# Optimization experiments

Measured on AMD Instinct MI355X. Metric: run time of the kernel, lower is better.

Reference implementation:

```python
import jax, jax.numpy as jnp
import numpy as np

K = 3          # kernel size
STRIDE = 2
PAD = 1
DIL = 1
SHAPE = 128    # input spatial extent per axis
B = 2          # batch size
N = 100000     # active input voxels
CIN = 32
COUT = 64
OUT = (SHAPE + 2 * PAD - DIL * (K - 1) - 1) // STRIDE + 1  # 64


def setup_inputs() -> dict:
    key = jax.random.key(0)
    kf, kw, kc, kb = jax.random.split(key, 4)
    features = jax.random.normal(kf, (N, CIN), jnp.float32)
    W = jax.random.normal(kw, (K, K, K, CIN, COUT), jnp.float32) * 0.05
    xyz = jax.random.randint(kc, (N, 3), 0, SHAPE, jnp.int32)
    b = jax.random.randint(kb, (N, 1), 0, B, jnp.int32)
    coors = jnp.concatenate([b, xyz], axis=1)  # [N, 4] = (batch, z, y, x)
    return {"features": features, "W": W, "coors": coors, "batch_size": B}


def reference(features, W, coors, batch_size):
    # Sparse 3D conv via gather-GEMM-scatter per kernel offset.
    # Output voxel o receives input p iff p = o*stride - pad + k*dil, i.e.
    # o = (p + pad - k*dil) / stride when divisible and in range.
    bidx = coors[:, 0].astype(jnp.int32)          # [N]
    pos = coors[:, 1:4].astype(jnp.int32)         # [N, 3]
    out = jnp.zeros((batch_size * OUT * OUT * OUT, COUT), features.dtype)
    for kz in range(K):
        for ky in range(K):
            for kx in range(K):
                off = jnp.array([kz, ky, kx], jnp.int32)
                num = pos + PAD - off * DIL        # [N, 3]
                o = num // STRIDE                  # candidate output coords
                valid = jnp.all((num % STRIDE == 0) & (o >= 0) & (o < OUT), axis=1)
                flat = ((bidx * OUT + o[:, 0]) * OUT + o[:, 1]) * OUT + o[:, 2]
                flat = jnp.where(valid, flat, 0)
                contrib = jnp.where(valid[:, None], features, 0.0) @ W[kz, ky, kx]
                out = out.at[flat].add(contrib)
    # Densified sparse-conv output: active sites hold exact spconv values,
    # inactive sites are zero (no contributions).
    return out.reshape(batch_size, OUT, OUT, OUT, COUT)
```

## Files before the change

kernel.cpp:

```cpp
#include <hip/hip_runtime.h>


#define CIN   32
#define COUT  64
#define OUTD  64
#define NBLK  2048
#define NPTS  128

__device__ __forceinline__ int axis_opts(int p, int* k, int* o) {
    int cnt = 0;
    const int kp = (p + 1) & 1;
    const int o0 = (p + 1 - kp) >> 1;
    if (o0 < OUTD) { k[cnt] = kp; o[cnt] = o0; ++cnt; }
    if (kp == 0) {
        const int o1 = o0 - 1;
        if (o1 >= 0) { k[cnt] = 2; o[cnt] = o1; ++cnt; }
    }
    return cnt;
}

__global__ void conv_w_bf16(const float* __restrict__ W, ushort* __restrict__ wsW)
{
    const int k = blockIdx.x;
    for (int i = threadIdx.x; i < CIN * COUT; i += 256) {
        const int c = i >> 6, ch = i & 63;
        const unsigned u = __float_as_uint(W[k * CIN * COUT + i]);
        const unsigned r = (u + 0x7fffu + ((u >> 16) & 1u)) >> 16;
        wsW[(k << 11) + (ch << 5) + c] = (ushort)r;
    }
}

__global__ __launch_bounds__(256) void scatter2(
    const float* __restrict__ feats, const ushort* __restrict__ wsW,
    const int4* __restrict__ coors, float* __restrict__ out,
    int N, int totWaves)
{
    const int ch = threadIdx.x & 63;
    const int wv = __builtin_amdgcn_readfirstlane(threadIdx.x >> 6);
    const int gwave = blockIdx.x * 4 + wv;

    for (int i = gwave; i < N; i += totWaves) {
        const int4 c = coors[i];
        const float4* fp = (const float4*)(feats + (size_t)i * CIN);
        float4 f[8];
        #pragma unroll
        for (int q = 0; q < 8; ++q) f[q] = fp[q];

        int kz[2], oz[2], ky[2], oy[2], kx[2], ox[2];
        const int nz = axis_opts(c.y, kz, oz);
        const int ny = axis_opts(c.z, ky, oy);
        const int nx = axis_opts(c.w, kx, ox);

        for (int az = 0; az < nz; ++az)
        for (int ay = 0; ay < ny; ++ay)
        for (int ax = 0; ax < nx; ++ax) {
            const int kidx = (kz[az] * 3 + ky[ay]) * 3 + kx[ax];
            const uint4* wp = (const uint4*)(wsW + (kidx << 11) + (ch << 5));
            uint4 w4[4];
            #pragma unroll
            for (int q = 0; q < 4; ++q) w4[q] = wp[q];
            float s0 = 0.f, s1 = 0.f;
            #pragma unroll
            for (int q = 0; q < 4; ++q) {
                const uint4 wq = w4[q];
                const float4 fa = f[2 * q], fb = f[2 * q + 1];
                s0 += fa.x * __uint_as_float(wq.x << 16);
                s1 += fa.y * __uint_as_float(wq.x & 0xffff0000u);
                s0 += fa.z * __uint_as_float(wq.y << 16);
                s1 += fa.w * __uint_as_float(wq.y & 0xffff0000u);
                s0 += fb.x * __uint_as_float(wq.z << 16);
                s1 += fb.y * __uint_as_float(wq.z & 0xffff0000u);
                s0 += fb.z * __uint_as_float(wq.w << 16);
                s1 += fb.w * __uint_as_float(wq.w & 0xffff0000u);
            }
            const size_t flat = (((size_t)c.x * OUTD + oz[az]) * OUTD + oy[ay]) * OUTD + ox[ax];
            unsafeAtomicAdd(out + flat * COUT + ch, s0 + s1);
        }
    }
}

__global__ __launch_bounds__(256, 4) void spconv_scatter(
    const float* __restrict__ feats, const float* __restrict__ Wt,
    const int* __restrict__ coors, float* __restrict__ out, int N)
{
    __shared__ float sf[NPTS][CIN];
    __shared__ int   sc[NPTS][4];
    __shared__ int   vf[NPTS];

    const int tid = threadIdx.x;
    const int ch  = tid & 63;
    const int wv  = tid >> 6;
    const int base = blockIdx.x * NPTS;
    const int npts = min(NPTS, (int)(N - base));
    if (npts <= 0) return;

    for (int i = tid; i < npts * CIN; i += 256) sf[0][i] = feats[base * CIN + i];
    for (int i = tid; i < npts * 4; i += 256) ((int*)sc)[i] = coors[base * 4 + i];
    __syncthreads();

    for (int off = 0; off < 27; ++off) {
        const int kz = off / 9, ky = (off / 3) % 3, kx = off % 3;
        if (tid < npts) {
            const int p  = tid;
            const int nz = sc[p][1] + 1 - kz;
            const int ny = sc[p][2] + 1 - ky;
            const int nx = sc[p][3] + 1 - kx;
            const int m  = nz | ny | nx;
            const int oz = nz >> 1, oy = ny >> 1, ox = nx >> 1;
            const bool v = ((m & 0x80000001) == 0) &&
                           (oz < OUTD) && (oy < OUTD) && (ox < OUTD);
            vf[p] = v ? (((sc[p][0] * OUTD + oz) * OUTD + oy) * OUTD + ox) : -1;
        }
        const float* wp = Wt + off * (CIN * COUT) + ch;
        float w[CIN];
        #pragma unroll
        for (int c = 0; c < CIN; ++c) w[c] = wp[c * COUT];
        __syncthreads();
        for (int p = wv; p < npts; p += 4) {
            const int f = vf[p];
            if (f >= 0) {
                float s = 0.f;
                #pragma unroll
                for (int c = 0; c < CIN; ++c) s += sf[p][c] * w[c];
                atomicAdd(&out[(size_t)f * COUT + ch], s);
            }
        }
        __syncthreads();
    }
}

extern "C" void kernel_launch(void* const* d_in, const int* in_sizes, int n_in,
                              void* d_out, int out_size, void* d_ws, size_t ws_size,
                              hipStream_t stream) {
    const float* feats = (const float*)d_in[0];
    const float* Wt    = (const float*)d_in[1];
    const int*   coors = (const int*)d_in[2];
    float*       out   = (float*)d_out;

    const int N = in_sizes[0] / CIN;

    hipMemsetAsync(d_out, 0, (size_t)out_size * sizeof(float), stream);

    const size_t need = 27 * CIN * COUT * sizeof(ushort);
    if (ws_size >= need) {
        ushort* wsW = (ushort*)d_ws;
        conv_w_bf16<<<27, 256, 0, stream>>>(Wt, wsW);
        const int NB = NBLK;
        scatter2<<<NB, 256, 0, stream>>>(feats, wsW, (const int4*)coors, out, N, NB * 4);
    } else {
        spconv_scatter<<<(N + NPTS - 1) / NPTS, 256, 0, stream>>>(feats, Wt, coors, out, N);
    }
}
```

Before: 133.5 us.

## Bin input-output pairs by kernel offset and scatter with fp32 register weights

Adds a binning pass that builds per-offset lists of (input, output) pairs, staged in LDS before a block-wide flush to global memory. A second kernel lets each wave take a 32-pair chunk of one offset, keep that offset's fp32 weights in registers, and run the dot products and atomic adds. This removes the per-pair bf16 weight reloads and the divergent per-point offset loops of the old path, and restores fp32 weights. In exchange it adds an extra kernel, an extra memset and pair traffic through global memory. The fixed per-offset capacity of 32768 pairs has no overflow check, which holds only for the expected point density.

```diff
diff --git a/kernel.cpp b/kernel.cpp
--- a/kernel.cpp
+++ b/kernel.cpp
@@ -1,11 +1,15 @@
 #include <hip/hip_runtime.h>
 
 
-#define CIN   32
-#define COUT  64
-#define OUTD  64
-#define NBLK  2048
-#define NPTS  128
+#define CIN    32
+#define COUT   64
+#define OUTD   64
+#define NBLK   2048
+#define NPTS   128
+#define BCAP   32768
+#define BINCAP 96
+#define CH     32
+#define NK     27
 
 __device__ __forceinline__ int axis_opts(int p, int* k, int* o) {
     int cnt = 0;
@@ -17,6 +21,102 @@
         if (o1 >= 0) { k[cnt] = 2; o[cnt] = o1; ++cnt; }
     }
     return cnt;
+}
+
+__global__ __launch_bounds__(256) void bin_pairs(
+    const int4* __restrict__ coors, int* __restrict__ gcur,
+    int2* __restrict__ pairs, int N)
+{
+    __shared__ int cntk[NK];
+    __shared__ int basek[NK];
+    __shared__ int li[NK * BINCAP];
+    __shared__ int lf[NK * BINCAP];
+
+    const int tid = threadIdx.x;
+    if (tid < NK) cntk[tid] = 0;
+    __syncthreads();
+
+    const int i = blockIdx.x * 256 + tid;
+    if (i < N) {
+        const int4 c = coors[i];
+        int kz[2], oz[2], ky[2], oy[2], kx[2], ox[2];
+        const int nz = axis_opts(c.y, kz, oz);
+        const int ny = axis_opts(c.z, ky, oy);
+        const int nx = axis_opts(c.w, kx, ox);
+        for (int az = 0; az < nz; ++az)
+        for (int ay = 0; ay < ny; ++ay)
+        for (int ax = 0; ax < nx; ++ax) {
+            const int kidx = (kz[az] * 3 + ky[ay]) * 3 + kx[ax];
+            const int flat = ((c.x * OUTD + oz[az]) * OUTD + oy[ay]) * OUTD + ox[ax];
+            const int slot = atomicAdd(&cntk[kidx], 1);
+            if (slot < BINCAP) {
+                li[kidx * BINCAP + slot] = i;
+                lf[kidx * BINCAP + slot] = flat;
+            } else {
+                const int pos = atomicAdd(&gcur[kidx], 1);
+                pairs[(size_t)kidx * BCAP + pos] = make_int2(i, flat);
+            }
+        }
+    }
+    __syncthreads();
+    if (tid < NK) basek[tid] = atomicAdd(&gcur[tid], min(cntk[tid], BINCAP));
+    __syncthreads();
+
+    for (int k = 0; k < NK; ++k) {
+        const int m = min(cntk[k], BINCAP);
+        const int base = basek[k];
+        for (int e = tid; e < m; e += 256)
+            pairs[(size_t)k * BCAP + base + e] = make_int2(li[k * BINCAP + e], lf[k * BINCAP + e]);
+    }
+}
+
+__global__ __launch_bounds__(256) void scatter_k(
+    const float* __restrict__ feats, const float* __restrict__ W,
+    const int* __restrict__ gcur, const int2* __restrict__ pairs,
+    float* __restrict__ out, int totWaves)
+{
+    const int ch = threadIdx.x & 63;
+    const int wv = threadIdx.x >> 6;
+    const int gwave = blockIdx.x * 4 + wv;
+
+    for (int v = gwave; ; v += totWaves) {
+        int rem = v, selk = -1, seloff = 0, selcnt = 0;
+        #pragma unroll
+        for (int k = 0; k < NK; ++k) {
+            const int cnt = gcur[k];
+            const int ck  = (cnt + CH - 1) >> 5;
+            if (selk < 0) {
+                if (rem < ck) { selk = k; seloff = rem << 5; selcnt = cnt; }
+                else rem -= ck;
+            }
+        }
+        if (selk < 0) break;
+
+        const float* wp = W + (selk << 11) + ch;
+        float w[CIN];
+        #pragma unroll
+        for (int c = 0; c < CIN; ++c) w[c] = wp[c << 6];
+
+        const int m = min(CH, selcnt - seloff);
+        const int2* pb = pairs + (size_t)selk * BCAP + seloff;
+        for (int e = 0; e < m; ++e) {
+            const int2 pr = pb[e];
+            const float4* fp = (const float4*)(feats + (size_t)pr.x * CIN);
+            float4 f[8];
+            #pragma unroll
+            for (int q = 0; q < 8; ++q) f[q] = fp[q];
+            float s0 = 0.f, s1 = 0.f, s2 = 0.f, s3 = 0.f;
+            #pragma unroll
+            for (int q = 0; q < 8; ++q) {
+                const float4 fq = f[q];
+                s0 += fq.x * w[4 * q + 0];
+                s1 += fq.y * w[4 * q + 1];
+                s2 += fq.z * w[4 * q + 2];
+                s3 += fq.w * w[4 * q + 3];
+            }
+            unsafeAtomicAdd(out + (size_t)pr.y * COUT + ch, (s0 + s1) + (s2 + s3));
+        }
+    }
 }
 
 __global__ void conv_w_bf16(const float* __restrict__ W, ushort* __restrict__ wsW)
@@ -141,12 +241,19 @@
 
     hipMemsetAsync(d_out, 0, (size_t)out_size * sizeof(float), stream);
 
-    const size_t need = 27 * CIN * COUT * sizeof(ushort);
-    if (ws_size >= need) {
+    const size_t needK = 32 * sizeof(int) + (size_t)NK * BCAP * sizeof(int2);
+    const size_t needB = 27 * CIN * COUT * sizeof(ushort);
+
+    if (ws_size >= needK) {
+        int*  gcur  = (int*)d_ws;
+        int2* pairs = (int2*)((char*)d_ws + 32 * sizeof(int));
+        hipMemsetAsync(gcur, 0, 32 * sizeof(int), stream);
+        bin_pairs<<<(N + 255) / 256, 256, 0, stream>>>((const int4*)coors, gcur, pairs, N);
+        scatter_k<<<NBLK, 256, 0, stream>>>(feats, Wt, gcur, pairs, out, NBLK * 4);
+    } else if (ws_size >= needB) {
         ushort* wsW = (ushort*)d_ws;
         conv_w_bf16<<<27, 256, 0, stream>>>(Wt, wsW);
-        const int NB = NBLK;
-        scatter2<<<NB, 256, 0, stream>>>(feats, wsW, (const int4*)coors, out, N, NB * 4);
+        scatter2<<<NBLK, 256, 0, stream>>>(feats, wsW, (const int4*)coors, out, N, NBLK * 4);
     } else {
         spconv_scatter<<<(N + NPTS - 1) / NPTS, 256, 0, stream>>>(feats, Wt, coors, out, N);
     }
```

Result: slower. 164.2 us (+23.0%).

## Replace scatter-atomic conv with dense voxel map and output-row gather kernel

Applied to the files above, without the earlier changes.

Builds a dense voxel-to-index hash map (with linked lists for duplicate coordinates) in workspace. A new kernel walks output rows: for each row it looks up the contributing input voxels through the map, accumulates into shared-memory tiles with LDS atomics, and writes every output value once. This removes both the separate memset of the 67MB output and the global atomics, at the cost of a 16MB map memset, per-block weight conversion, and irregular linked-list traversal.

```diff
diff --git a/kernel.cpp b/kernel.cpp
--- a/kernel.cpp
+++ b/kernel.cpp
@@ -4,30 +4,180 @@
 #define CIN   32
 #define COUT  64
 #define OUTD  64
+#define IND   128
+#define RPB   4
+#define NTH   512
+#define WSTR  20
+#define NPTS  128
 #define NBLK  2048
-#define NPTS  128
+
+__global__ void build_map(const int4* __restrict__ coors, int* __restrict__ map,
+                          int* __restrict__ nxt, int N)
+{
+    int i = blockIdx.x * 256 + threadIdx.x;
+    if (i >= N) return;
+    const int4 c = coors[i];
+    const int v = ((c.x * IND + c.y) * IND + c.z) * IND + c.w;
+    nxt[i] = atomicExch(&map[v], i);
+}
+
+__global__ __launch_bounds__(NTH) void row_gather(
+    const float* __restrict__ feats, const float* __restrict__ W,
+    const int* __restrict__ map, const int* __restrict__ nxt,
+    float* __restrict__ out)
+{
+    __shared__ __align__(16) float    accf[RPB * 64 * COUT];
+    __shared__ __align__(16) unsigned wfu[3 * 64 * WSTR];
+
+    const int tid = threadIdx.x;
+    const int ch  = tid & 63;
+    const int wv  = tid >> 6;
+    const int row0 = blockIdx.x * RPB;
+    const int b   = row0 >> 12;
+    const int oz  = (row0 >> 6) & 63;
+    const int oy0 = row0 & 63;
+
+    for (int i = tid; i < RPB * 64 * COUT; i += NTH) accf[i] = 0.f;
+
+    for (int s = 0; s < 9; ++s) {
+        const int kz = s / 3, ky = s % 3;
+        const int pz = 2 * oz - 1 + kz;
+        const bool sv = ((unsigned)pz < IND);
+        __syncthreads();
+
+        if (sv) {
+            const float* Ws = W + ((kz * 3 + ky) * 3) * (CIN * COUT);
+            for (int i = tid; i < 3 * 64 * 16; i += NTH) {
+                const int chh = i & 63;
+                const int cp  = (i >> 6) & 15;
+                const int kx  = i >> 10;
+                const unsigned u0 = __float_as_uint(Ws[kx * 2048 + (2 * cp) * 64 + chh]);
+                const unsigned u1 = __float_as_uint(Ws[kx * 2048 + (2 * cp + 1) * 64 + chh]);
+                const unsigned b0 = (u0 + 0x7fffu + ((u0 >> 16) & 1u)) >> 16;
+                const unsigned b1 = (u1 + 0x7fffu + ((u1 >> 16) & 1u)) >> 16;
+                wfu[(kx * 64 + chh) * WSTR + cp] = b0 | (b1 << 16);
+            }
+        }
+        __syncthreads();
+        if (!sv) continue;
+
+        for (int r = 0; r < RPB; ++r) {
+            const int py = 2 * (oy0 + r) - 1 + ky;
+            if ((unsigned)py >= IND) continue;
+            const int* rowp = map + ((b * IND + pz) * IND + py) * IND;
+            const int2 mv = ((const int2*)rowp)[ch];
+            const unsigned long long bE = __ballot(mv.x >= 0);
+            const unsigned long long bO = __ballot(mv.y >= 0);
+            int cnt = 0;
+
+            for (unsigned long long m = bE; m; m &= m - 1, ++cnt) {
+                if ((cnt & 7) != wv) continue;
+                const int L = __builtin_ctzll(m);
+                int j = __shfl(mv.x, L);
+                while (j >= 0) {
+                    const float4* fp = (const float4*)(feats + (size_t)j * CIN);
+                    float4 f[8];
+                    #pragma unroll
+                    for (int q = 0; q < 8; ++q) f[q] = fp[q];
+                    {
+                        const uint4* wq = (const uint4*)(wfu + (1 * 64 + ch) * WSTR);
+                        float s0 = 0.f, s1 = 0.f;
+                        #pragma unroll
+                        for (int q = 0; q < 4; ++q) {
+                            const uint4 w4 = wq[q];
+                            const float4 fa = f[2 * q], fb = f[2 * q + 1];
+                            s0 += fa.x * __uint_as_float(w4.x << 16);
+                            s1 += fa.y * __uint_as_float(w4.x & 0xffff0000u);
+                            s0 += fa.z * __uint_as_float(w4.y << 16);
+                            s1 += fa.w * __uint_as_float(w4.y & 0xffff0000u);
+                            s0 += fb.x * __uint_as_float(w4.z << 16);
+                            s1 += fb.y * __uint_as_float(w4.z & 0xffff0000u);
+                            s0 += fb.z * __uint_as_float(w4.w << 16);
+                            s1 += fb.w * __uint_as_float(w4.w & 0xffff0000u);
+                        }
+                        unsafeAtomicAdd(&accf[(r * 64 + L) * COUT + ch], s0 + s1);
+                    }
+                    j = nxt[j];
+                }
+            }
+            for (unsigned long long m = bO; m; m &= m - 1, ++cnt) {
+                if ((cnt & 7) != wv) continue;
+                const int L = __builtin_ctzll(m);
+                int j = __shfl(mv.y, L);
+                while (j >= 0) {
+                    const float4* fp = (const float4*)(feats + (size_t)j * CIN);
+                    float4 f[8];
+                    #pragma unroll
+                    for (int q = 0; q < 8; ++q) f[q] = fp[q];
+                    {
+                        const uint4* wq = (const uint4*)(wfu + (2 * 64 + ch) * WSTR);
+                        float s0 = 0.f, s1 = 0.f;
+                        #pragma unroll
+                        for (int q = 0; q < 4; ++q) {
+                            const uint4 w4 = wq[q];
+                            const float4 fa = f[2 * q], fb = f[2 * q + 1];
+                            s0 += fa.x * __uint_as_float(w4.x << 16);
+                            s1 += fa.y * __uint_as_float(w4.x & 0xffff0000u);
+                            s0 += fa.z * __uint_as_float(w4.y << 16);
+                            s1 += fa.w * __uint_as_float(w4.y & 0xffff0000u);
+                            s0 += fb.x * __uint_as_float(w4.z << 16);
+                            s1 += fb.y * __uint_as_float(w4.z & 0xffff0000u);
+                            s0 += fb.z * __uint_as_float(w4.w << 16);
+                            s1 += fb.w * __uint_as_float(w4.w & 0xffff0000u);
+                        }
+                        unsafeAtomicAdd(&accf[(r * 64 + L) * COUT + ch], s0 + s1);
+                    }
+                    if (L < 63) {
+                        const uint4* wq = (const uint4*)(wfu + (0 * 64 + ch) * WSTR);
+                        float s0 = 0.f, s1 = 0.f;
+                        #pragma unroll
+                        for (int q = 0; q < 4; ++q) {
+                            const uint4 w4 = wq[q];
+                            const float4 fa = f[2 * q], fb = f[2 * q + 1];
+                            s0 += fa.x * __uint_as_float(w4.x << 16);
+                            s1 += fa.y * __uint_as_float(w4.x & 0xffff0000u);
+                            s0 += fa.z * __uint_as_float(w4.y << 16);
+                            s1 += fa.w * __uint_as_float(w4.y & 0xffff0000u);
+                            s0 += fb.x * __uint_as_float(w4.z << 16);
+                            s1 += fb.y * __uint_as_float(w4.z & 0xffff0000u);
+                            s0 += fb.z * __uint_as_float(w4.w << 16);
+                            s1 += fb.w * __uint_as_float(w4.w & 0xffff0000u);
+                        }
+                        unsafeAtomicAdd(&accf[(r * 64 + L + 1) * COUT + ch], s0 + s1);
+                    }
+                    j = nxt[j];
+                }
+            }
+        }
+    }
+    __syncthreads();
+
+    float* op = out + (size_t)row0 * (64 * COUT);
+    #pragma unroll
+    for (int it = 0; it < 8; ++it) {
+        const int i = (it * NTH + tid) * 4;
+        *(float4*)(op + i) = *(const float4*)(accf + i);
+    }
+}
+
+__global__ void conv_w_bf16(const float* __restrict__ W, ushort* __restrict__ wsW)
+{
+    const int k = blockIdx.x;
+    for (int i = threadIdx.x; i < CIN * COUT; i += 256) {
+        const int c = i >> 6, chh = i & 63;
+        const unsigned u = __float_as_uint(W[k * CIN * COUT + i]);
+        const unsigned r = (u + 0x7fffu + ((u >> 16) & 1u)) >> 16;
+        wsW[(k << 11) + (chh << 5) + c] = (ushort)r;
+    }
+}
 
 __device__ __forceinline__ int axis_opts(int p, int* k, int* o) {
     int cnt = 0;
     const int kp = (p + 1) & 1;
     const int o0 = (p + 1 - kp) >> 1;
     if (o0 < OUTD) { k[cnt] = kp; o[cnt] = o0; ++cnt; }
-    if (kp == 0) {
-        const int o1 = o0 - 1;
-        if (o1 >= 0) { k[cnt] = 2; o[cnt] = o1; ++cnt; }
-    }
+    if (kp == 0) { const int o1 = o0 - 1; if (o1 >= 0) { k[cnt] = 2; o[cnt] = o1; ++cnt; } }
     return cnt;
-}
-
-__global__ void conv_w_bf16(const float* __restrict__ W, ushort* __restrict__ wsW)
-{
-    const int k = blockIdx.x;
-    for (int i = threadIdx.x; i < CIN * COUT; i += 256) {
-        const int c = i >> 6, ch = i & 63;
-        const unsigned u = __float_as_uint(W[k * CIN * COUT + i]);
-        const unsigned r = (u + 0x7fffu + ((u >> 16) & 1u)) >> 16;
-        wsW[(k << 11) + (ch << 5) + c] = (ushort)r;
-    }
 }
 
 __global__ __launch_bounds__(256) void scatter2(
@@ -35,27 +185,24 @@
     const int4* __restrict__ coors, float* __restrict__ out,
     int N, int totWaves)
 {
-    const int ch = threadIdx.x & 63;
+    const int chh = threadIdx.x & 63;
     const int wv = __builtin_amdgcn_readfirstlane(threadIdx.x >> 6);
     const int gwave = blockIdx.x * 4 + wv;
-
     for (int i = gwave; i < N; i += totWaves) {
         const int4 c = coors[i];
         const float4* fp = (const float4*)(feats + (size_t)i * CIN);
         float4 f[8];
         #pragma unroll
         for (int q = 0; q < 8; ++q) f[q] = fp[q];
-
         int kz[2], oz[2], ky[2], oy[2], kx[2], ox[2];
         const int nz = axis_opts(c.y, kz, oz);
         const int ny = axis_opts(c.z, ky, oy);
         const int nx = axis_opts(c.w, kx, ox);
-
         for (int az = 0; az < nz; ++az)
         for (int ay = 0; ay < ny; ++ay)
         for (int ax = 0; ax < nx; ++ax) {
             const int kidx = (kz[az] * 3 + ky[ay]) * 3 + kx[ax];
-            const uint4* wp = (const uint4*)(wsW + (kidx << 11) + (ch << 5));
+            const uint4* wp = (const uint4*)(wsW + (kidx << 11) + (chh << 5));
             uint4 w4[4];
             #pragma unroll
             for (int q = 0; q < 4; ++q) w4[q] = wp[q];
@@ -74,7 +221,7 @@
                 s1 += fb.w * __uint_as_float(wq.w & 0xffff0000u);
             }
             const size_t flat = (((size_t)c.x * OUTD + oz[az]) * OUTD + oy[ay]) * OUTD + ox[ax];
-            unsafeAtomicAdd(out + flat * COUT + ch, s0 + s1);
+            unsafeAtomicAdd(out + flat * COUT + chh, s0 + s1);
         }
     }
 }
@@ -86,18 +233,15 @@
     __shared__ float sf[NPTS][CIN];
     __shared__ int   sc[NPTS][4];
     __shared__ int   vf[NPTS];
-
     const int tid = threadIdx.x;
-    const int ch  = tid & 63;
+    const int chh = tid & 63;
     const int wv  = tid >> 6;
     const int base = blockIdx.x * NPTS;
-    const int npts = min(NPTS, (int)(N - base));
+    const int npts = min(NPTS, (int)(blockIdx.x * NPTS < N ? N - base : 0));
     if (npts <= 0) return;
-
     for (int i = tid; i < npts * CIN; i += 256) sf[0][i] = feats[base * CIN + i];
     for (int i = tid; i < npts * 4; i += 256) ((int*)sc)[i] = coors[base * 4 + i];
     __syncthreads();
-
     for (int off = 0; off < 27; ++off) {
         const int kz = off / 9, ky = (off / 3) % 3, kx = off % 3;
         if (tid < npts) {
@@ -111,7 +255,7 @@
                            (oz < OUTD) && (oy < OUTD) && (ox < OUTD);
             vf[p] = v ? (((sc[p][0] * OUTD + oz) * OUTD + oy) * OUTD + ox) : -1;
         }
-        const float* wp = Wt + off * (CIN * COUT) + ch;
+        const float* wp = Wt + off * (CIN * COUT) + chh;
         float w[CIN];
         #pragma unroll
         for (int c = 0; c < CIN; ++c) w[c] = wp[c * COUT];
@@ -122,7 +266,7 @@
                 float s = 0.f;
                 #pragma unroll
                 for (int c = 0; c < CIN; ++c) s += sf[p][c] * w[c];
-                atomicAdd(&out[(size_t)f * COUT + ch], s);
+                atomicAdd(&out[(size_t)f * COUT + chh], s);
             }
         }
         __syncthreads();
@@ -138,16 +282,26 @@
     float*       out   = (float*)d_out;
 
     const int N = in_sizes[0] / CIN;
-
-    hipMemsetAsync(d_out, 0, (size_t)out_size * sizeof(float), stream);
-
-    const size_t need = 27 * CIN * COUT * sizeof(ushort);
-    if (ws_size >= need) {
+    const int B = out_size / (OUTD * OUTD * OUTD * COUT);
+
+    const size_t mapElems = (size_t)B * IND * IND * IND;
+    const size_t needMap  = (mapElems + (size_t)N) * sizeof(int);
+    const size_t needBf   = 27 * CIN * COUT * sizeof(ushort);
+
+    if (ws_size >= needMap) {
+        int* map = (int*)d_ws;
+        int* nxt = map + mapElems;
+        hipMemsetAsync(map, 0xFF, mapElems * sizeof(int), stream);
+        build_map<<<(N + 255) / 256, 256, 0, stream>>>((const int4*)coors, map, nxt, N);
+        const int nRows = B * OUTD * OUTD;
+        row_gather<<<nRows / RPB, NTH, 0, stream>>>(feats, Wt, map, nxt, out);
+    } else if (ws_size >= needBf) {
+        hipMemsetAsync(d_out, 0, (size_t)out_size * sizeof(float), stream);
         ushort* wsW = (ushort*)d_ws;
         conv_w_bf16<<<27, 256, 0, stream>>>(Wt, wsW);
-        const int NB = NBLK;
-        scatter2<<<NB, 256, 0, stream>>>(feats, wsW, (const int4*)coors, out, N, NB * 4);
+        scatter2<<<NBLK, 256, 0, stream>>>(feats, wsW, (const int4*)coors, out, N, NBLK * 4);
     } else {
+        hipMemsetAsync(d_out, 0, (size_t)out_size * sizeof(float), stream);
         spconv_scatter<<<(N + NPTS - 1) / NPTS, 256, 0, stream>>>(feats, Wt, coors, out, N);
     }
 }
```

Result: slower. 286.8 us (+114.9%).

## Replace atomic scatter with tiled gather using dense voxel hash map

Applied to the files above, without the earlier changes.

Builds a dense per-batch voxel index map with chained duplicates, then has each block own a 4x4x4 output tile, gather contributing inputs from the map, accumulate in LDS with shared atomics, and write the tile out densely. This removes the separate output memset and the global float atomics of the scatter path, and caches all 27 bf16-packed weights in LDS. The cost is a 2*128^3 int map memset plus build, reconverting weights per block, and a fixed CAP of 512 entries per tile that silently drops contributions if exceeded.

```diff
diff --git a/kernel.cpp b/kernel.cpp
--- a/kernel.cpp
+++ b/kernel.cpp
@@ -4,18 +4,144 @@
 #define CIN   32
 #define COUT  64
 #define OUTD  64
+#define IND   128
+#define TILE  4
+#define NTILE 16
+#define NTH   512
+#define GRID  1024
+#define CAP   512
+#define NPTS  128
 #define NBLK  2048
-#define NPTS  128
+
+__global__ void build_map(const int4* __restrict__ coors, int* __restrict__ map,
+                          int* __restrict__ nxt, int N)
+{
+    int i = blockIdx.x * 256 + threadIdx.x;
+    if (i >= N) return;
+    const int4 c = coors[i];
+    const int v = ((c.x * IND + c.y) * IND + c.z) * IND + c.w;
+    nxt[i] = atomicExch(&map[v], i);
+}
+
+__global__ __launch_bounds__(NTH) void gather_p(
+    const float* __restrict__ feats, const float* __restrict__ W,
+    const int* __restrict__ map, const int* __restrict__ nxt,
+    float* __restrict__ out, int nT)
+{
+    __shared__ unsigned wfu[27 * 16 * 64];
+    __shared__ float    accf[TILE*TILE*TILE*COUT];
+    __shared__ int      list[CAP];
+    __shared__ int      cnt;
+
+    const int tid = threadIdx.x;
+    const int ch  = tid & 63;
+    const int wv  = tid >> 6;
+
+    for (int i = tid; i < 27 * 16 * 64; i += NTH) {
+        const int chh = i & 63, cp = (i >> 6) & 15, k = i >> 10;
+        const float* Ws = W + k * 2048 + (2 * cp) * 64 + chh;
+        const unsigned u0 = __float_as_uint(Ws[0]);
+        const unsigned u1 = __float_as_uint(Ws[64]);
+        const unsigned b0 = (u0 + 0x7fffu + ((u0 >> 16) & 1u)) >> 16;
+        const unsigned b1 = (u1 + 0x7fffu + ((u1 >> 16) & 1u)) >> 16;
+        wfu[i] = b0 | (b1 << 16);
+    }
+    for (int i = tid; i < TILE*TILE*TILE*COUT; i += NTH) accf[i] = 0.f;
+    if (tid == 0) cnt = 0;
+
+    for (int tile = blockIdx.x; tile < nT; tile += GRID) {
+        int t = tile;
+        const int ox0 = (t & 15) * TILE; t >>= 4;
+        const int oy0 = (t & 15) * TILE; t >>= 4;
+        const int oz0 = (t & 15) * TILE; t >>= 4;
+        const int b   = t;
+        __syncthreads();
+
+        const int mapBase = b * IND * IND * IND;
+        for (int idx = tid; idx < 9 * 9 * 9; idx += NTH) {
+            const int rx = idx % 9, ry = (idx / 9) % 9, rz = idx / 81;
+            const int px = 2 * ox0 - 1 + rx;
+            const int py = 2 * oy0 - 1 + ry;
+            const int pz = 2 * oz0 - 1 + rz;
+            if ((unsigned)px >= IND || (unsigned)py >= IND || (unsigned)pz >= IND) continue;
+            int j = map[mapBase + (pz * IND + py) * IND + px];
+            if (j < 0) continue;
+
+            const int kpx = (px + 1) & 1, ox1 = (px + 1 - kpx) >> 1;
+            const int kpy = (py + 1) & 1, oy1 = (py + 1 - kpy) >> 1;
+            const int kpz = (pz + 1) & 1, oz1 = (pz + 1 - kpz) >> 1;
+
+            bool ok[8]; int pre[8];
+            #pragma unroll
+            for (int cz = 0; cz < 2; ++cz)
+            #pragma unroll
+            for (int cy = 0; cy < 2; ++cy)
+            #pragma unroll
+            for (int cx = 0; cx < 2; ++cx) {
+                const int kz = kpz + 2 * cz, ky = kpy + 2 * cy, kx = kpx + 2 * cx;
+                const int olz = oz1 - cz - oz0, oly = oy1 - cy - oy0, olx = ox1 - cx - ox0;
+                const int ci = (cz * 2 + cy) * 2 + cx;
+                ok[ci]  = (kz <= 2) && (ky <= 2) && (kx <= 2) &&
+                          ((unsigned)olz < TILE) && ((unsigned)oly < TILE) &&
+                          ((unsigned)olx < TILE);
+                pre[ci] = (((kz * 3 + ky) * 3 + kx) << 6) | ((olz * TILE + oly) * TILE + olx);
+            }
+            for (; j >= 0; j = nxt[j]) {
+                #pragma unroll
+                for (int ci = 0; ci < 8; ++ci) {
+                    if (ok[ci]) {
+                        const int s = atomicAdd(&cnt, 1);
+                        if (s < CAP) list[s] = (j << 11) | pre[ci];
+                    }
+                }
+            }
+        }
+        __syncthreads();
+
+        const int m = min(cnt, CAP);
+        #pragma unroll 2
+        for (int i = wv; i < m; i += 8) {
+            const int e = list[i];
+            const int vox = e & 63, k = (e >> 6) & 31, j = e >> 11;
+            const float4* fp = (const float4*)(feats + (size_t)j * CIN);
+            float4 f[8];
+            #pragma unroll
+            for (int q = 0; q < 8; ++q) f[q] = fp[q];
+            const float2* g = (const float2*)f;
+            const unsigned* wb = wfu + (k << 10) + ch;
+            float s0 = 0.f, s1 = 0.f;
+            #pragma unroll
+            for (int cp = 0; cp < 16; ++cp) {
+                const unsigned u = wb[cp << 6];
+                const float2 gq = g[cp];
+                s0 += gq.x * __uint_as_float(u << 16);
+                s1 += gq.y * __uint_as_float(u & 0xffff0000u);
+            }
+            unsafeAtomicAdd(&accf[vox * COUT + ch], s0 + s1);
+        }
+        __syncthreads();
+
+        #pragma unroll
+        for (int it = 0; it < 2; ++it) {
+            const int i4 = (it * NTH + tid) * 4;
+            float4 v = *(float4*)(accf + i4);
+            *(float4*)(accf + i4) = make_float4(0.f, 0.f, 0.f, 0.f);
+            const int row = i4 >> 8;
+            const int vz = row >> 2, vy = row & 3;
+            const int inrow = i4 & 255;
+            const size_t gidx = ((((size_t)b * OUTD + (oz0 + vz)) * OUTD + (oy0 + vy)) * OUTD + ox0) * COUT + inrow;
+            *(float4*)(out + gidx) = v;
+        }
+        if (tid == 0) cnt = 0;
+    }
+}
 
 __device__ __forceinline__ int axis_opts(int p, int* k, int* o) {
     int cnt = 0;
     const int kp = (p + 1) & 1;
     const int o0 = (p + 1 - kp) >> 1;
     if (o0 < OUTD) { k[cnt] = kp; o[cnt] = o0; ++cnt; }
-    if (kp == 0) {
-        const int o1 = o0 - 1;
-        if (o1 >= 0) { k[cnt] = 2; o[cnt] = o1; ++cnt; }
-    }
+    if (kp == 0) { const int o1 = o0 - 1; if (o1 >= 0) { k[cnt] = 2; o[cnt] = o1; ++cnt; } }
     return cnt;
 }
 
@@ -23,10 +149,10 @@
 {
     const int k = blockIdx.x;
     for (int i = threadIdx.x; i < CIN * COUT; i += 256) {
-        const int c = i >> 6, ch = i & 63;
+        const int c = i >> 6, chh = i & 63;
         const unsigned u = __float_as_uint(W[k * CIN * COUT + i]);
         const unsigned r = (u + 0x7fffu + ((u >> 16) & 1u)) >> 16;
-        wsW[(k << 11) + (ch << 5) + c] = (ushort)r;
+        wsW[(k << 11) + (chh << 5) + c] = (ushort)r;
     }
 }
 
@@ -35,27 +161,24 @@
     const int4* __restrict__ coors, float* __restrict__ out,
     int N, int totWaves)
 {
-    const int ch = threadIdx.x & 63;
+    const int chh = threadIdx.x & 63;
     const int wv = __builtin_amdgcn_readfirstlane(threadIdx.x >> 6);
     const int gwave = blockIdx.x * 4 + wv;
-
     for (int i = gwave; i < N; i += totWaves) {
         const int4 c = coors[i];
         const float4* fp = (const float4*)(feats + (size_t)i * CIN);
         float4 f[8];
         #pragma unroll
         for (int q = 0; q < 8; ++q) f[q] = fp[q];
-
         int kz[2], oz[2], ky[2], oy[2], kx[2], ox[2];
         const int nz = axis_opts(c.y, kz, oz);
         const int ny = axis_opts(c.z, ky, oy);
         const int nx = axis_opts(c.w, kx, ox);
-
         for (int az = 0; az < nz; ++az)
         for (int ay = 0; ay < ny; ++ay)
         for (int ax = 0; ax < nx; ++ax) {
             const int kidx = (kz[az] * 3 + ky[ay]) * 3 + kx[ax];
-            const uint4* wp = (const uint4*)(wsW + (kidx << 11) + (ch << 5));
+            const uint4* wp = (const uint4*)(wsW + (kidx << 11) + (chh << 5));
             uint4 w4[4];
             #pragma unroll
             for (int q = 0; q < 4; ++q) w4[q] = wp[q];
@@ -74,7 +197,7 @@
                 s1 += fb.w * __uint_as_float(wq.w & 0xffff0000u);
             }
             const size_t flat = (((size_t)c.x * OUTD + oz[az]) * OUTD + oy[ay]) * OUTD + ox[ax];
-            unsafeAtomicAdd(out + flat * COUT + ch, s0 + s1);
+            unsafeAtomicAdd(out + flat * COUT + chh, s0 + s1);
         }
     }
 }
@@ -86,18 +209,15 @@
     __shared__ float sf[NPTS][CIN];
     __shared__ int   sc[NPTS][4];
     __shared__ int   vf[NPTS];
-
     const int tid = threadIdx.x;
-    const int ch  = tid & 63;
+    const int chh = tid & 63;
     const int wv  = tid >> 6;
     const int base = blockIdx.x * NPTS;
     const int npts = min(NPTS, (int)(N - base));
     if (npts <= 0) return;
-
     for (int i = tid; i < npts * CIN; i += 256) sf[0][i] = feats[base * CIN + i];
     for (int i = tid; i < npts * 4; i += 256) ((int*)sc)[i] = coors[base * 4 + i];
     __syncthreads();
-
     for (int off = 0; off < 27; ++off) {
         const int kz = off / 9, ky = (off / 3) % 3, kx = off % 3;
         if (tid < npts) {
@@ -111,7 +231,7 @@
                            (oz < OUTD) && (oy < OUTD) && (ox < OUTD);
             vf[p] = v ? (((sc[p][0] * OUTD + oz) * OUTD + oy) * OUTD + ox) : -1;
         }
-        const float* wp = Wt + off * (CIN * COUT) + ch;
+        const float* wp = Wt + off * (CIN * COUT) + chh;
         float w[CIN];
         #pragma unroll
         for (int c = 0; c < CIN; ++c) w[c] = wp[c * COUT];
@@ -122,7 +242,7 @@
                 float s = 0.f;
                 #pragma unroll
                 for (int c = 0; c < CIN; ++c) s += sf[p][c] * w[c];
-                atomicAdd(&out[(size_t)f * COUT + ch], s);
+                atomicAdd(&out[(size_t)f * COUT + chh], s);
             }
         }
         __syncthreads();
@@ -138,16 +258,26 @@
     float*       out   = (float*)d_out;
 
     const int N = in_sizes[0] / CIN;
-
-    hipMemsetAsync(d_out, 0, (size_t)out_size * sizeof(float), stream);
-
-    const size_t need = 27 * CIN * COUT * sizeof(ushort);
-    if (ws_size >= need) {
+    const int B = out_size / (OUTD * OUTD * OUTD * COUT);
+
+    const size_t mapElems = (size_t)B * IND * IND * IND;
+    const size_t needMap  = (mapElems + (size_t)N) * sizeof(int);
+    const size_t needBf   = 27 * CIN * COUT * sizeof(ushort);
+
+    if (ws_size >= needMap) {
+        int* map = (int*)d_ws;
+        int* nxt = map + mapElems;
+        hipMemsetAsync(map, 0xFF, mapElems * sizeof(int), stream);
+        build_map<<<(N + 255) / 256, 256, 0, stream>>>((const int4*)coors, map, nxt, N);
+        const int nT = B * NTILE * NTILE * NTILE;
+        gather_p<<<GRID, NTH, 0, stream>>>(feats, Wt, map, nxt, out, nT);
+    } else if (ws_size >= needBf) {
+        hipMemsetAsync(d_out, 0, (size_t)out_size * sizeof(float), stream);
         ushort* wsW = (ushort*)d_ws;
         conv_w_bf16<<<27, 256, 0, stream>>>(Wt, wsW);
-        const int NB = NBLK;
-        scatter2<<<NB, 256, 0, stream>>>(feats, wsW, (const int4*)coors, out, N, NB * 4);
+        scatter2<<<NBLK, 256, 0, stream>>>(feats, wsW, (const int4*)coors, out, N, NBLK * 4);
     } else {
+        hipMemsetAsync(d_out, 0, (size_t)out_size * sizeof(float), stream);
         spconv_scatter<<<(N + NPTS - 1) / NPTS, 256, 0, stream>>>(feats, Wt, coors, out, N);
     }
 }
```

Result: slower. 301.1 us (+125.6%).
